# Kernel tuning notes

Hardware: AMD Instinct MI355X
Metric: run time of the kernel (lower is better)

## Reference

```python
import jax, jax.numpy as jnp
import numpy as np

N = 50000
E = 800000
NFEAT = 128
NHID = 32
HEADS = 8
NCLASS = 40


def _gat_conv(x, src, dst, W, att_src, att_dst, bias, concat):
    # x: [N, Fin]; W: [Fin, H*C]; att_*: [H, C]; bias: [H*C] or [C]
    n = x.shape[0]
    H, C = att_src.shape
    h = (x @ W).reshape(n, H, C)                      # [N,H,C]
    a_src = (h * att_src[None]).sum(-1)               # [N,H]
    a_dst = (h * att_dst[None]).sum(-1)               # [N,H]
    e = jax.nn.leaky_relu(a_src[src] + a_dst[dst], 0.2)  # [E,H]
    # edge softmax over incoming edges of each dst node
    m = jax.ops.segment_max(e, dst, num_segments=n)   # [N,H]
    e = jnp.exp(e - m[dst])
    s = jax.ops.segment_sum(e, dst, num_segments=n)   # [N,H]
    alpha = e / (s[dst] + 1e-16)                      # [E,H]
    msg = h[src] * alpha[:, :, None]                  # [E,H,C]
    out = jax.ops.segment_sum(msg, dst, num_segments=n)  # [N,H,C]
    if concat:
        out = out.reshape(n, H * C)
    else:
        out = out.mean(axis=1)
    return out + bias


def setup_inputs() -> dict:
    key = jax.random.key(0)
    ks = jax.random.split(key, 10)
    x = jax.random.normal(ks[0], (N, NFEAT), dtype=jnp.float32)
    edge_index = jax.random.randint(ks[1], (2, E), 0, N, dtype=jnp.int64)
    sc = 1.0 / np.sqrt(NFEAT)
    W1 = jax.random.uniform(ks[2], (NFEAT, HEADS * NHID), jnp.float32, -sc, sc)
    a1_src = jax.random.uniform(ks[3], (HEADS, NHID), jnp.float32, -sc, sc)
    a1_dst = jax.random.uniform(ks[4], (HEADS, NHID), jnp.float32, -sc, sc)
    b1 = jnp.zeros((HEADS * NHID,), jnp.float32)
    sc2 = 1.0 / np.sqrt(HEADS * NHID)
    W2 = jax.random.uniform(ks[5], (HEADS * NHID, NCLASS), jnp.float32, -sc2, sc2)
    a2_src = jax.random.uniform(ks[6], (1, NCLASS), jnp.float32, -sc2, sc2)
    a2_dst = jax.random.uniform(ks[7], (1, NCLASS), jnp.float32, -sc2, sc2)
    b2 = jnp.zeros((NCLASS,), jnp.float32)
    return {"x": x, "edge_index": edge_index, "W1": W1, "a1_src": a1_src,
            "a1_dst": a1_dst, "b1": b1, "W2": W2, "a2_src": a2_src,
            "a2_dst": a2_dst, "b2": b2}


def reference(x, edge_index, W1, a1_src, a1_dst, b1, W2, a2_src, a2_dst, b2):
    n = x.shape[0]
    loop = jnp.arange(n, dtype=edge_index.dtype)
    src = jnp.concatenate([edge_index[0], loop])  # add self-loops (PyG default)
    dst = jnp.concatenate([edge_index[1], loop])
    # dropout layers are identity in eval mode
    h = jax.nn.elu(_gat_conv(x, src, dst, W1, a1_src, a1_dst, b1, concat=True))
    out = _gat_conv(h, src, dst, W2, a2_src, a2_dst, b2, concat=False)
    return jax.nn.log_softmax(out, axis=1)
```

## Files before the change

kernel.cpp:

```cpp
#include <hip/hip_runtime.h>
#include <math.h>

#define NFEAT  128
#define HC     256
#define HEADS  8
#define NHID   32
#define NCLASS 40

typedef unsigned int  uint;
typedef unsigned short ushort;
typedef unsigned char uchar;

typedef __attribute__((ext_vector_type(8))) short bf16x8;
typedef __attribute__((ext_vector_type(4))) float f32x4;

union U8 { uint4 u; bf16x8 v; };

__device__ __forceinline__ uint f2bf1(float f) {
    uint b = __float_as_uint(f);
    b += 0x7FFFu + ((b >> 16) & 1u);
    return b >> 16;
}
__device__ __forceinline__ uint packbf(float lo, float hi) {
    return f2bf1(lo) | (f2bf1(hi) << 16);
}
__device__ __forceinline__ float bflo(uint u) { return __uint_as_float(u << 16); }
__device__ __forceinline__ float bfhi(uint u) { return __uint_as_float(u & 0xFFFF0000u); }

__device__ __forceinline__ uchar f2fp8(float v) {
    return (uchar)(__builtin_amdgcn_cvt_pk_fp8_f32(v, v, 0, false) & 0xFF);
}
__device__ __forceinline__ float fp8tof(uint byte) {
    auto v2 = __builtin_amdgcn_cvt_pk_f32_fp8((int)byte, false);
    return v2[0];
}


#define HU 8
#define PREPB 23
__global__ __launch_bounds__(256)
void k_hist_prep(const int* __restrict__ dst, int E, int* deg,
                 int* __restrict__ rank,
                 const float* __restrict__ W1,
                 const float* __restrict__ attS, const float* __restrict__ attD,
                 const float* __restrict__ W2,
                 const float* __restrict__ a2sw, const float* __restrict__ a2dw,
                 ushort* __restrict__ Wb1, ushort* __restrict__ Wb2) {
    int blk = blockIdx.x;
    int t = threadIdx.x;
    if (blk >= PREPB) {
        int tid = (blk - PREPB) * 256 + t;
        int stride = (gridDim.x - PREPB) * 256;
#pragma unroll
        for (int j = 0; j < HU; ++j) {
            int i = tid + j * stride;
            if (i < E) rank[i] = atomicAdd(&deg[dst[i]], 1);
        }
        return;
    }
    float f[8];
    if (blk < 17) {
        int g = blk * 256 + t;
        int lane = g & 63;
        int step = (g >> 6) & 3;
        int tile = g >> 8;
        int k0 = step * 32 + (lane >> 4) * 8;
        if (tile < 16) {
            int ncol = tile * 16 + (lane & 15);
#pragma unroll
            for (int j = 0; j < 8; ++j) f[j] = W1[(size_t)(k0 + j) * HC + ncol];
        } else {
            int cc = lane & 15;
            int h = cc & 7;
            const float* av = (cc < 8) ? attS : attD;
#pragma unroll
            for (int j = 0; j < 8; ++j) {
                const float* wr = W1 + (size_t)(k0 + j) * HC + h * 32;
                float s = 0.f;
#pragma unroll
                for (int c = 0; c < 32; ++c) s += wr[c] * av[h * 32 + c];
                f[j] = s;
            }
        }
        uint4 o;
        o.x = packbf(f[0], f[1]);
        o.y = packbf(f[2], f[3]);
        o.z = packbf(f[4], f[5]);
        o.w = packbf(f[6], f[7]);
        *(uint4*)(Wb1 + (size_t)g * 8) = o;
    } else {
        int g = (blk - 17) * 256 + t;
        if (g >= 3 * 8 * 64) return;
        int lane = g & 63;
        int ks = (g >> 6) & 7;
        int nt = g >> 9;
        int cc = lane & 15;
        int ncol = nt * 16 + cc;
        int k0 = ks * 32 + (lane >> 4) * 8;
        if (ncol < NCLASS) {
#pragma unroll
            for (int j = 0; j < 8; ++j) f[j] = W2[(size_t)(k0 + j) * NCLASS + ncol];
        } else if (ncol <= 41) {
            const float* av = (ncol == 40) ? a2sw : a2dw;
#pragma unroll
            for (int j = 0; j < 8; ++j) {
                const float* wr = W2 + (size_t)(k0 + j) * NCLASS;
                float s = 0.f;
#pragma unroll
                for (int c = 0; c < NCLASS; ++c) s += wr[c] * av[c];
                f[j] = s;
            }
        } else {
#pragma unroll
            for (int j = 0; j < 8; ++j) f[j] = 0.f;
        }
        uint4 o;
        o.x = packbf(f[0], f[1]);
        o.y = packbf(f[2], f[3]);
        o.z = packbf(f[4], f[5]);
        o.w = packbf(f[6], f[7]);
        *(uint4*)(Wb2 + (size_t)g * 8) = o;
    }
}

__global__ void k_blocksum(const int* __restrict__ deg, int n, int* bsum) {
    __shared__ int lds[256];
    int b = blockIdx.x, t = threadIdx.x;
    int i = b * 256 + t;
    lds[t] = (i < n) ? deg[i] + 1 : 0;
    __syncthreads();
    for (int off = 128; off >= 1; off >>= 1) {
        if (t < off) lds[t] += lds[t + off];
        __syncthreads();
    }
    if (t == 0) bsum[b] = lds[0];
}

__global__ void k_mkptr(const int* __restrict__ deg, const int* __restrict__ bsum,
                        int n, int* ptr) {
    __shared__ int lds[256];
    __shared__ int base_s;
    int b = blockIdx.x, t = threadIdx.x;
    int p = 0;
    for (int i = t; i < b; i += 256) p += bsum[i];
    lds[t] = p;
    __syncthreads();
    for (int off = 128; off >= 1; off >>= 1) {
        if (t < off) lds[t] += lds[t + off];
        __syncthreads();
    }
    if (t == 0) base_s = lds[0];
    __syncthreads();
    int i = b * 256 + t;
    int v = (i < n) ? deg[i] + 1 : 0;
    lds[t] = v;
    __syncthreads();
    for (int off = 1; off < 256; off <<= 1) {
        int u = (t >= off) ? lds[t - off] : 0;
        __syncthreads();
        lds[t] += u;
        __syncthreads();
    }
    int excl = lds[t] - v + base_s;
    if (i < n) {
        ptr[i] = excl;
        if (i == n - 1) ptr[n] = excl + v;
    }
}

#define SU 4
__global__ __launch_bounds__(256)
void k_scatter_gemm1(const int* __restrict__ srcE, const int* __restrict__ dstE,
                     const int* __restrict__ rank, const int* __restrict__ ptr,
                     int E, int n, int* __restrict__ srcs, int scb,
                     const float* __restrict__ x, const ushort* __restrict__ Wb,
                     uchar* __restrict__ h1f8, float* __restrict__ a1x) {
    __shared__ uint Xs[64 * 68];
    int t = threadIdx.x;
    if (blockIdx.x < scb) {
        int tid = blockIdx.x * 256 + t;
        int stride = scb * 256;
        int tot = E + n;
#pragma unroll
        for (int j = 0; j < SU; ++j) {
            int i = tid + j * stride;
            if (i >= tot) continue;
            if (i < E) {
                int d = dstE[i];
                srcs[ptr[d] + rank[i]] = srcE[i];
            } else {
                int v = i - E;
                srcs[ptr[v + 1] - 1] = v;
            }
        }
        return;
    }
    int lane = t & 63;
    int w = t >> 6;
    int n0 = (blockIdx.x - scb) * 64;

#pragma unroll
    for (int j = 0; j < 8; ++j) {
        int f4 = t + j * 256;
        int node = f4 >> 5;
        int k4 = (f4 & 31) * 4;
        int gn = n0 + node;
        float4 v = make_float4(0.f, 0.f, 0.f, 0.f);
        if (gn < n) v = *(const float4*)(x + (size_t)gn * NFEAT + k4);
        uint2 pk;
        pk.x = packbf(v.x, v.y);
        pk.y = packbf(v.z, v.w);
        *(uint2*)(Xs + node * 68 + (k4 >> 1)) = pk;
    }
    __syncthreads();

    int m = lane & 15;
    int q4 = (lane >> 4) * 4;
    bf16x8 Af[4];
#pragma unroll
    for (int ks = 0; ks < 4; ++ks) {
        U8 a;
        a.u = *(const uint4*)(Xs + (w * 16 + m) * 68 + ks * 16 + q4);
        Af[ks] = a.v;
    }
    __syncthreads();

    f32x4 acc[17];
#pragma unroll
    for (int i = 0; i < 17; ++i) acc[i] = (f32x4){0.f, 0.f, 0.f, 0.f};

    const bf16x8* Bf = (const bf16x8*)Wb;
#pragma unroll
    for (int ks = 0; ks < 4; ++ks) {
#pragma unroll
        for (int nt = 0; nt < 17; ++nt) {
            bf16x8 bv = Bf[(size_t)(nt * 4 + ks) * 64 + lane];
            acc[nt] = __builtin_amdgcn_mfma_f32_16x16x32_bf16(Af[ks], bv, acc[nt], 0, 0, 0);
        }
    }

    int cc = lane & 15;
    int r0 = (lane >> 4) * 4;

#pragma unroll
    for (int r = 0; r < 4; ++r) {
        int gn = n0 + w * 16 + r0 + r;
        if (gn < n) a1x[(size_t)gn * 16 + cc] = acc[16][r];
    }

    uchar* CsB = (uchar*)Xs;
#pragma unroll
    for (int nt = 0; nt < 16; ++nt) {
#pragma unroll
        for (int r = 0; r < 4; ++r)
            CsB[(w * 16 + r0 + r) * 272 + nt * 16 + cc] = f2fp8(acc[nt][r]);
    }
    __syncthreads();

    int node_local = t >> 2;
    int q = t & 3;
    int gn = n0 + node_local;
    if (gn < n) {
        const uchar* crow = CsB + node_local * 272 + q * 64;
        uchar* hp = h1f8 + (size_t)gn * HC + q * 64;
#pragma unroll
        for (int i = 0; i < 4; ++i)
            *(uint4*)(hp + i * 16) = *(const uint4*)(crow + i * 16);
    }
}

__global__ __launch_bounds__(256)
void k_agg1(const uint* __restrict__ h1u, const float* __restrict__ a1x,
            const float* __restrict__ b1,
            const int* __restrict__ ptr, const int* __restrict__ srcs,
            int n, ushort* __restrict__ hgb) {
    int wid = blockIdx.x * 4 + (threadIdx.x >> 6);
    if (wid >= n) return;
    int lane = threadIdx.x & 63;
    int h = lane >> 3;
    float adn = a1x[(size_t)wid * 16 + 8 + h];
    int beg = __builtin_amdgcn_readfirstlane(ptr[wid]);
    int end = __builtin_amdgcn_readfirstlane(ptr[wid + 1]);
    float m = -INFINITY, s = 0.f;
    float4 acc = make_float4(0.f, 0.f, 0.f, 0.f);

    int i = beg;
    for (; i + 8 <= end; i += 8) {
        int sn[8];
#pragma unroll
        for (int j = 0; j < 8; ++j) sn[j] = __builtin_amdgcn_readfirstlane(srcs[i + j]);
        float av[8];
        uint hv[8];
#pragma unroll
        for (int j = 0; j < 8; ++j) av[j] = a1x[(size_t)sn[j] * 16 + h];
#pragma unroll
        for (int j = 0; j < 8; ++j)
            hv[j] = h1u[(size_t)sn[j] * 64 + lane];
        float e[8];
#pragma unroll
        for (int j = 0; j < 8; ++j) {
            float a = av[j] + adn;
            e[j] = (a > 0.f) ? a : 0.2f * a;
        }
        float mn = m;
#pragma unroll
        for (int j = 0; j < 8; ++j) mn = fmaxf(mn, e[j]);
        float corr = __expf(m - mn);
        float p[8];
#pragma unroll
        for (int j = 0; j < 8; ++j) p[j] = __expf(e[j] - mn);
        float ps = 0.f;
#pragma unroll
        for (int j = 0; j < 8; ++j) ps += p[j];
        s = s * corr + ps;
        float cx = acc.x * corr, cy = acc.y * corr, cz = acc.z * corr, cw = acc.w * corr;
#pragma unroll
        for (int j = 0; j < 8; ++j) {
            auto lo = __builtin_amdgcn_cvt_pk_f32_fp8((int)hv[j], false);
            auto hi = __builtin_amdgcn_cvt_pk_f32_fp8((int)hv[j], true);
            cx += p[j] * lo[0];
            cy += p[j] * lo[1];
            cz += p[j] * hi[0];
            cw += p[j] * hi[1];
        }
        acc = make_float4(cx, cy, cz, cw);
        m = mn;
    }
    if (i < end) {
        int sn[8];
        bool val[8];
#pragma unroll
        for (int j = 0; j < 8; ++j) {
            int idx = i + j;
            val[j] = idx < end;
            sn[j] = __builtin_amdgcn_readfirstlane(srcs[val[j] ? idx : end - 1]);
        }
        float av[8];
        uint hv[8];
#pragma unroll
        for (int j = 0; j < 8; ++j) av[j] = a1x[(size_t)sn[j] * 16 + h];
#pragma unroll
        for (int j = 0; j < 8; ++j)
            hv[j] = h1u[(size_t)sn[j] * 64 + lane];
        float e[8];
#pragma unroll
        for (int j = 0; j < 8; ++j) {
            float a = av[j] + adn;
            e[j] = val[j] ? ((a > 0.f) ? a : 0.2f * a) : -INFINITY;
        }
        float mn = m;
#pragma unroll
        for (int j = 0; j < 8; ++j) mn = fmaxf(mn, e[j]);
        float corr = __expf(m - mn);
        float p[8];
#pragma unroll
        for (int j = 0; j < 8; ++j) p[j] = __expf(e[j] - mn);
        float ps = 0.f;
#pragma unroll
        for (int j = 0; j < 8; ++j) ps += p[j];
        s = s * corr + ps;
        float cx = acc.x * corr, cy = acc.y * corr, cz = acc.z * corr, cw = acc.w * corr;
#pragma unroll
        for (int j = 0; j < 8; ++j) {
            auto lo = __builtin_amdgcn_cvt_pk_f32_fp8((int)hv[j], false);
            auto hi = __builtin_amdgcn_cvt_pk_f32_fp8((int)hv[j], true);
            cx += p[j] * lo[0];
            cy += p[j] * lo[1];
            cz += p[j] * hi[0];
            cw += p[j] * hi[1];
        }
        acc = make_float4(cx, cy, cz, cw);
        m = mn;
    }

    float inv = 1.f / (s + 1e-16f);
    float4 bv = *(const float4*)(b1 + lane * 4);
    float4 o;
    o.x = acc.x * inv + bv.x;
    o.y = acc.y * inv + bv.y;
    o.z = acc.z * inv + bv.z;
    o.w = acc.w * inv + bv.w;
    o.x = (o.x > 0.f) ? o.x : (__expf(o.x) - 1.f);
    o.y = (o.y > 0.f) ? o.y : (__expf(o.y) - 1.f);
    o.z = (o.z > 0.f) ? o.z : (__expf(o.z) - 1.f);
    o.w = (o.w > 0.f) ? o.w : (__expf(o.w) - 1.f);
    uint2 ov;
    ov.x = packbf(o.x, o.y);
    ov.y = packbf(o.z, o.w);
    *(uint2*)(hgb + (size_t)wid * HC + lane * 4) = ov;
}

__global__ __launch_bounds__(256)
void k_gemm2(const ushort* __restrict__ hgb, const ushort* __restrict__ Wb2,
             int n, uchar* __restrict__ h2f8) {
    __shared__ uint Xs[64 * 132];
    int t = threadIdx.x;
    int lane = t & 63;
    int w = t >> 6;
    int n0 = blockIdx.x * 64;

#pragma unroll
    for (int j = 0; j < 8; ++j) {
        int g = t + j * 256;
        int node = g >> 5;
        int u4 = g & 31;
        int gn = n0 + node;
        uint4 v = make_uint4(0u, 0u, 0u, 0u);
        if (gn < n) v = *(const uint4*)(hgb + (size_t)gn * HC + u4 * 8);
        *(uint4*)(Xs + node * 132 + u4 * 4) = v;
    }
    __syncthreads();

    int m = lane & 15;
    int q4 = (lane >> 4) * 4;
    bf16x8 Af[8];
#pragma unroll
    for (int ks = 0; ks < 8; ++ks) {
        U8 a;
        a.u = *(const uint4*)(Xs + (w * 16 + m) * 132 + ks * 16 + q4);
        Af[ks] = a.v;
    }
    __syncthreads();

    f32x4 acc[3];
#pragma unroll
    for (int i = 0; i < 3; ++i) acc[i] = (f32x4){0.f, 0.f, 0.f, 0.f};

    const bf16x8* Bf = (const bf16x8*)Wb2;
#pragma unroll
    for (int ks = 0; ks < 8; ++ks) {
#pragma unroll
        for (int nt = 0; nt < 3; ++nt) {
            bf16x8 bv = Bf[(size_t)(nt * 8 + ks) * 64 + lane];
            acc[nt] = __builtin_amdgcn_mfma_f32_16x16x32_bf16(Af[ks], bv, acc[nt], 0, 0, 0);
        }
    }

    int cc = lane & 15;
    int r0 = (lane >> 4) * 4;

    uchar* CsB = (uchar*)Xs;
#pragma unroll
    for (int nt = 0; nt < 2; ++nt) {
#pragma unroll
        for (int r = 0; r < 4; ++r)
            CsB[(w * 16 + r0 + r) * 64 + nt * 16 + cc] = f2fp8(acc[nt][r]);
    }
#pragma unroll
    for (int r = 0; r < 4; ++r) {
        int row = (w * 16 + r0 + r) * 64;
        if (cc < 8)       CsB[row + 32 + cc] = f2fp8(acc[2][r]);
        else if (cc == 8) *(float*)(CsB + row + 40) = acc[2][r];
        else if (cc == 9) *(float*)(CsB + row + 44) = acc[2][r];
        else if (cc == 10) *(uint*)(CsB + row + 48) = 0u;
        else if (cc == 11) *(uint*)(CsB + row + 52) = 0u;
        else if (cc == 12) *(uint*)(CsB + row + 56) = 0u;
        else if (cc == 13) *(uint*)(CsB + row + 60) = 0u;
    }
    __syncthreads();

    int node_local = t >> 2;
    int q = t & 3;
    int gn = n0 + node_local;
    if (gn < n)
        *(uint4*)(h2f8 + (size_t)gn * 64 + q * 16) =
            *(const uint4*)(CsB + node_local * 64 + q * 16);
}

__global__ __launch_bounds__(256)
void k_agg2(const uchar* __restrict__ h2f8, const float* __restrict__ b2,
            const int* __restrict__ ptr, const int* __restrict__ srcs,
            int n, float* __restrict__ out) {
    int wid = blockIdx.x * 4 + (threadIdx.x >> 6);
    if (wid >= n) return;
    int lane = threadIdx.x & 63;
    bool live = lane < NCLASS;
    int col = live ? lane : 0;
    float adn = *(const float*)(h2f8 + (size_t)wid * 64 + 44);
    int beg = __builtin_amdgcn_readfirstlane(ptr[wid]);
    int end = __builtin_amdgcn_readfirstlane(ptr[wid + 1]);
    float m = -INFINITY, s = 0.f, acc = 0.f;

    int i = beg;
    for (; i + 8 <= end; i += 8) {
        int sn[8];
#pragma unroll
        for (int j = 0; j < 8; ++j) sn[j] = __builtin_amdgcn_readfirstlane(srcs[i + j]);
        float av[8];
        uint hb[8];
#pragma unroll
        for (int j = 0; j < 8; ++j)
            av[j] = *(const float*)(h2f8 + (size_t)sn[j] * 64 + 40);
#pragma unroll
        for (int j = 0; j < 8; ++j)
            hb[j] = h2f8[(size_t)sn[j] * 64 + col];
        float e[8];
#pragma unroll
        for (int j = 0; j < 8; ++j) {
            float a = av[j] + adn;
            e[j] = (a > 0.f) ? a : 0.2f * a;
        }
        float mn = m;
#pragma unroll
        for (int j = 0; j < 8; ++j) mn = fmaxf(mn, e[j]);
        float corr = __expf(m - mn);
        float p[8];
#pragma unroll
        for (int j = 0; j < 8; ++j) p[j] = __expf(e[j] - mn);
        float ps = 0.f, pa = 0.f;
#pragma unroll
        for (int j = 0; j < 8; ++j) { ps += p[j]; pa += p[j] * fp8tof(hb[j]); }
        s = s * corr + ps;
        acc = acc * corr + pa;
        m = mn;
    }
    if (i < end) {
        int sn[8];
        bool val[8];
#pragma unroll
        for (int j = 0; j < 8; ++j) {
            int idx = i + j;
            val[j] = idx < end;
            sn[j] = __builtin_amdgcn_readfirstlane(srcs[val[j] ? idx : end - 1]);
        }
        float av[8];
        uint hb[8];
#pragma unroll
        for (int j = 0; j < 8; ++j)
            av[j] = *(const float*)(h2f8 + (size_t)sn[j] * 64 + 40);
#pragma unroll
        for (int j = 0; j < 8; ++j)
            hb[j] = h2f8[(size_t)sn[j] * 64 + col];
        float e[8];
#pragma unroll
        for (int j = 0; j < 8; ++j) {
            float a = av[j] + adn;
            e[j] = val[j] ? ((a > 0.f) ? a : 0.2f * a) : -INFINITY;
        }
        float mn = m;
#pragma unroll
        for (int j = 0; j < 8; ++j) mn = fmaxf(mn, e[j]);
        float corr = __expf(m - mn);
        float p[8];
#pragma unroll
        for (int j = 0; j < 8; ++j) p[j] = __expf(e[j] - mn);
        float ps = 0.f, pa = 0.f;
#pragma unroll
        for (int j = 0; j < 8; ++j) { ps += p[j]; pa += p[j] * fp8tof(hb[j]); }
        s = s * corr + ps;
        acc = acc * corr + pa;
        m = mn;
    }

    float val0 = acc / (s + 1e-16f) + (live ? b2[lane] : 0.f);
    float vmax = live ? val0 : -INFINITY;
#pragma unroll
    for (int msk = 1; msk < 64; msk <<= 1) vmax = fmaxf(vmax, __shfl_xor(vmax, msk, 64));
    float ex = live ? __expf(val0 - vmax) : 0.f;
#pragma unroll
    for (int msk = 1; msk < 64; msk <<= 1) ex += __shfl_xor(ex, msk, 64);
    float res = val0 - vmax - __logf(ex);
    if (live) out[(size_t)wid * NCLASS + lane] = res;
}

extern "C" void kernel_launch(void* const* d_in, const int* in_sizes, int n_in,
                              void* d_out, int out_size, void* d_ws, size_t ws_size,
                              hipStream_t stream) {
    const float* x    = (const float*)d_in[0];
    const int*   ei   = (const int*)  d_in[1];
    const float* W1   = (const float*)d_in[2];
    const float* attS = (const float*)d_in[3];
    const float* attD = (const float*)d_in[4];
    const float* b1   = (const float*)d_in[5];
    const float* W2   = (const float*)d_in[6];
    const float* a2sw = (const float*)d_in[7];
    const float* a2dw = (const float*)d_in[8];
    const float* b2   = (const float*)d_in[9];

    int n = in_sizes[0] / NFEAT;
    int E = in_sizes[1] / 2;
    const int* srcE = ei;
    const int* dstE = ei + E;
    int nb = (n + 255) / 256;
    int mblocks = (n + 63) / 64;

    char* p = (char*)d_ws;
    auto alloc = [&](size_t bytes) {
        char* r = p;
        p += (bytes + 255) & ~(size_t)255;
        return r;
    };
    uchar*  h1f8 = (uchar*)alloc((size_t)n * HC);
    ushort* hgb  = (ushort*)alloc((size_t)n * HC * 2);
    uchar*  h2f8 = (uchar*)alloc((size_t)n * 64);
    ushort* Wb1  = (ushort*)alloc((size_t)17 * 4 * 64 * 8 * 2);
    ushort* Wb2  = (ushort*)alloc((size_t)3 * 8 * 64 * 8 * 2);
    float* a1x = (float*)alloc((size_t)n * 16 * 4);
    int* deg  = (int*)alloc((size_t)n * 4);
    int* rank = (int*)alloc((size_t)E * 4);
    int* bsum = (int*)alloc((size_t)nb * 4);
    int* ptr  = (int*)alloc((size_t)(n + 1) * 4);
    int* srcs = (int*)alloc((size_t)(E + n) * 4);

    int tot = E + n;
    int histb = (E + 256 * HU - 1) / (256 * HU);
    int scb = (tot + 256 * SU - 1) / (256 * SU);
    hipMemsetAsync(deg, 0, (size_t)n * 4, stream);
    k_hist_prep<<<PREPB + histb, 256, 0, stream>>>(dstE, E, deg, rank,
                                                   W1, attS, attD, W2, a2sw, a2dw,
                                                   Wb1, Wb2);
    k_blocksum<<<nb, 256, 0, stream>>>(deg, n, bsum);
    k_mkptr<<<nb, 256, 0, stream>>>(deg, bsum, n, ptr);

    k_scatter_gemm1<<<scb + mblocks, 256, 0, stream>>>(
        srcE, dstE, rank, ptr, E, n, srcs, scb, x, Wb1, h1f8, a1x);

    k_agg1<<<(n + 3) / 4, 256, 0, stream>>>((const uint*)h1f8, a1x, b1,
                                            ptr, srcs, n, hgb);
    k_gemm2<<<(n + 63) / 64, 256, 0, stream>>>(hgb, Wb2, n, h2f8);
    k_agg2<<<(n + 3) / 4, 256, 0, stream>>>(h2f8, b2, ptr, srcs, n, (float*)d_out);
}
```

Measured before the change: 251.0 us.

## Distribute edge softmax across lanes with bpermute reductions and exp2 prescaling

```diff
diff --git a/kernel.cpp b/kernel.cpp
--- a/kernel.cpp
+++ b/kernel.cpp
@@ -7,6 +7,8 @@
 #define NHID   32
 #define NCLASS 40
 
+#define INV_LN2 1.44269504088896340736f
+
 typedef unsigned int  uint;
 typedef unsigned short ushort;
 typedef unsigned char uchar;
@@ -33,6 +35,10 @@
 __device__ __forceinline__ float fp8tof(uint byte) {
     auto v2 = __builtin_amdgcn_cvt_pk_f32_fp8((int)byte, false);
     return v2[0];
+}
+
+__device__ __forceinline__ float bperm(int addr, float v) {
+    return __int_as_float(__builtin_amdgcn_ds_bpermute(addr, __float_as_int(v)));
 }
 
 
@@ -79,7 +85,7 @@
                 float s = 0.f;
 #pragma unroll
                 for (int c = 0; c < 32; ++c) s += wr[c] * av[h * 32 + c];
-                f[j] = s;
+                f[j] = s * INV_LN2;
             }
         }
         uint4 o;
@@ -108,7 +114,7 @@
                 float s = 0.f;
 #pragma unroll
                 for (int c = 0; c < NCLASS; ++c) s += wr[c] * av[c];
-                f[j] = s;
+                f[j] = s * INV_LN2;
             }
         } else {
 #pragma unroll
@@ -277,109 +283,69 @@
     int wid = blockIdx.x * 4 + (threadIdx.x >> 6);
     if (wid >= n) return;
     int lane = threadIdx.x & 63;
-    int h = lane >> 3;
-    float adn = a1x[(size_t)wid * 16 + 8 + h];
+    int vj = lane >> 3;
+    int hh = lane & 7;
+    int hacc = lane >> 3;
+    float adn = a1x[(size_t)wid * 16 + 8 + hh];
+    const char* a1xb = (const char*)a1x;
+    const char* srcsb = (const char*)srcs;
+    int ax8  = (lane ^ 8)  << 2;
+    int ax16 = (lane ^ 16) << 2;
+    int ax32 = (lane ^ 32) << 2;
+    int bpc  = hacc << 2;
+    int bpp[8];
+#pragma unroll
+    for (int j = 0; j < 8; ++j) bpp[j] = ((j << 3) + hacc) << 2;
+
     int beg = __builtin_amdgcn_readfirstlane(ptr[wid]);
     int end = __builtin_amdgcn_readfirstlane(ptr[wid + 1]);
     float m = -INFINITY, s = 0.f;
     float4 acc = make_float4(0.f, 0.f, 0.f, 0.f);
 
-    int i = beg;
-    for (; i + 8 <= end; i += 8) {
-        int sn[8];
-#pragma unroll
-        for (int j = 0; j < 8; ++j) sn[j] = __builtin_amdgcn_readfirstlane(srcs[i + j]);
-        float av[8];
-        uint hv[8];
-#pragma unroll
-        for (int j = 0; j < 8; ++j) av[j] = a1x[(size_t)sn[j] * 16 + h];
-#pragma unroll
-        for (int j = 0; j < 8; ++j)
-            hv[j] = h1u[(size_t)sn[j] * 64 + lane];
-        float e[8];
+    for (int i = beg; i < end; i += 8) {
+        int idx = i + vj;
+        bool valid = idx < end;
+        int ci = valid ? idx : (end - 1);
+        int sv = *(const int*)(srcsb + ((uint)ci << 2));
+        float av = *(const float*)(a1xb + ((uint)sv << 6) + ((uint)hh << 2));
+        float a = av + adn;
+        float e = fmaxf(a, 0.2f * a);
+        e = valid ? e : -INFINITY;
+        float em = fmaxf(e, bperm(ax8, e));
+        em = fmaxf(em, bperm(ax16, em));
+        em = fmaxf(em, bperm(ax32, em));
+        float mn = fmaxf(m, em);
+        float corr = __builtin_exp2f(m - mn);
+        float p = __builtin_exp2f(e - mn);
+        float ps = p + bperm(ax8, p);
+        ps += bperm(ax16, ps);
+        ps += bperm(ax32, ps);
+        s = s * corr + ps;
+        m = mn;
+        float corr_a = bperm(bpc, corr);
+        acc.x *= corr_a; acc.y *= corr_a; acc.z *= corr_a; acc.w *= corr_a;
 #pragma unroll
         for (int j = 0; j < 8; ++j) {
-            float a = av[j] + adn;
-            e[j] = (a > 0.f) ? a : 0.2f * a;
-        }
-        float mn = m;
-#pragma unroll
-        for (int j = 0; j < 8; ++j) mn = fmaxf(mn, e[j]);
-        float corr = __expf(m - mn);
-        float p[8];
-#pragma unroll
-        for (int j = 0; j < 8; ++j) p[j] = __expf(e[j] - mn);
-        float ps = 0.f;
-#pragma unroll
-        for (int j = 0; j < 8; ++j) ps += p[j];
-        s = s * corr + ps;
-        float cx = acc.x * corr, cy = acc.y * corr, cz = acc.z * corr, cw = acc.w * corr;
-#pragma unroll
-        for (int j = 0; j < 8; ++j) {
-            auto lo = __builtin_amdgcn_cvt_pk_f32_fp8((int)hv[j], false);
-            auto hi = __builtin_amdgcn_cvt_pk_f32_fp8((int)hv[j], true);
-            cx += p[j] * lo[0];
-            cy += p[j] * lo[1];
-            cz += p[j] * hi[0];
-            cw += p[j] * hi[1];
-        }
-        acc = make_float4(cx, cy, cz, cw);
-        m = mn;
-    }
-    if (i < end) {
-        int sn[8];
-        bool val[8];
-#pragma unroll
-        for (int j = 0; j < 8; ++j) {
-            int idx = i + j;
-            val[j] = idx < end;
-            sn[j] = __builtin_amdgcn_readfirstlane(srcs[val[j] ? idx : end - 1]);
-        }
-        float av[8];
-        uint hv[8];
-#pragma unroll
-        for (int j = 0; j < 8; ++j) av[j] = a1x[(size_t)sn[j] * 16 + h];
-#pragma unroll
-        for (int j = 0; j < 8; ++j)
-            hv[j] = h1u[(size_t)sn[j] * 64 + lane];
-        float e[8];
-#pragma unroll
-        for (int j = 0; j < 8; ++j) {
-            float a = av[j] + adn;
-            e[j] = val[j] ? ((a > 0.f) ? a : 0.2f * a) : -INFINITY;
-        }
-        float mn = m;
-#pragma unroll
-        for (int j = 0; j < 8; ++j) mn = fmaxf(mn, e[j]);
-        float corr = __expf(m - mn);
-        float p[8];
-#pragma unroll
-        for (int j = 0; j < 8; ++j) p[j] = __expf(e[j] - mn);
-        float ps = 0.f;
-#pragma unroll
-        for (int j = 0; j < 8; ++j) ps += p[j];
-        s = s * corr + ps;
-        float cx = acc.x * corr, cy = acc.y * corr, cz = acc.z * corr, cw = acc.w * corr;
-#pragma unroll
-        for (int j = 0; j < 8; ++j) {
-            auto lo = __builtin_amdgcn_cvt_pk_f32_fp8((int)hv[j], false);
-            auto hi = __builtin_amdgcn_cvt_pk_f32_fp8((int)hv[j], true);
-            cx += p[j] * lo[0];
-            cy += p[j] * lo[1];
-            cz += p[j] * hi[0];
-            cw += p[j] * hi[1];
-        }
-        acc = make_float4(cx, cy, cz, cw);
-        m = mn;
+            int snj = __builtin_amdgcn_readlane(sv, 8 * j);
+            uint hv = h1u[(size_t)snj * 64 + lane];
+            float pj = bperm(bpp[j], p);
+            auto lo = __builtin_amdgcn_cvt_pk_f32_fp8((int)hv, false);
+            auto hi = __builtin_amdgcn_cvt_pk_f32_fp8((int)hv, true);
+            acc.x += pj * lo[0];
+            acc.y += pj * lo[1];
+            acc.z += pj * hi[0];
+            acc.w += pj * hi[1];
+        }
     }
 
     float inv = 1.f / (s + 1e-16f);
+    float inv_a = bperm(bpc, inv);
     float4 bv = *(const float4*)(b1 + lane * 4);
     float4 o;
-    o.x = acc.x * inv + bv.x;
-    o.y = acc.y * inv + bv.y;
-    o.z = acc.z * inv + bv.z;
-    o.w = acc.w * inv + bv.w;
+    o.x = acc.x * inv_a + bv.x;
+    o.y = acc.y * inv_a + bv.y;
+    o.z = acc.z * inv_a + bv.z;
+    o.w = acc.w * inv_a + bv.w;
     o.x = (o.x > 0.f) ? o.x : (__expf(o.x) - 1.f);
     o.y = (o.y > 0.f) ? o.y : (__expf(o.y) - 1.f);
     o.z = (o.z > 0.f) ? o.z : (__expf(o.z) - 1.f);
@@ -474,82 +440,51 @@
     int wid = blockIdx.x * 4 + (threadIdx.x >> 6);
     if (wid >= n) return;
     int lane = threadIdx.x & 63;
+    int vj = lane & 7;
     bool live = lane < NCLASS;
     int col = live ? lane : 0;
-    float adn = *(const float*)(h2f8 + (size_t)wid * 64 + 44);
+    const char* h2b = (const char*)h2f8;
+    const char* srcsb = (const char*)srcs;
+    float adn = *(const float*)(h2b + (size_t)wid * 64 + 44);
+    int ax1 = (lane ^ 1) << 2;
+    int ax2 = (lane ^ 2) << 2;
+    int ax4 = (lane ^ 4) << 2;
+    int bpj[8];
+#pragma unroll
+    for (int j = 0; j < 8; ++j) bpj[j] = j << 2;
+
     int beg = __builtin_amdgcn_readfirstlane(ptr[wid]);
     int end = __builtin_amdgcn_readfirstlane(ptr[wid + 1]);
     float m = -INFINITY, s = 0.f, acc = 0.f;
 
-    int i = beg;
-    for (; i + 8 <= end; i += 8) {
-        int sn[8];
-#pragma unroll
-        for (int j = 0; j < 8; ++j) sn[j] = __builtin_amdgcn_readfirstlane(srcs[i + j]);
-        float av[8];
-        uint hb[8];
-#pragma unroll
-        for (int j = 0; j < 8; ++j)
-            av[j] = *(const float*)(h2f8 + (size_t)sn[j] * 64 + 40);
-#pragma unroll
-        for (int j = 0; j < 8; ++j)
-            hb[j] = h2f8[(size_t)sn[j] * 64 + col];
-        float e[8];
+    for (int i = beg; i < end; i += 8) {
+        int idx = i + vj;
+        bool valid = idx < end;
+        int ci = valid ? idx : (end - 1);
+        int sv = *(const int*)(srcsb + ((uint)ci << 2));
+        float av = *(const float*)(h2b + ((uint)sv << 6) + 40u);
+        float a = av + adn;
+        float e = fmaxf(a, 0.2f * a);
+        e = valid ? e : -INFINITY;
+        float em = fmaxf(e, bperm(ax1, e));
+        em = fmaxf(em, bperm(ax2, em));
+        em = fmaxf(em, bperm(ax4, em));
+        float mn = fmaxf(m, em);
+        float corr = __builtin_exp2f(m - mn);
+        float p = __builtin_exp2f(e - mn);
+        float ps = p + bperm(ax1, p);
+        ps += bperm(ax2, ps);
+        ps += bperm(ax4, ps);
+        s = s * corr + ps;
+        acc = acc * corr;
+        m = mn;
 #pragma unroll
         for (int j = 0; j < 8; ++j) {
-            float a = av[j] + adn;
-            e[j] = (a > 0.f) ? a : 0.2f * a;
-        }
-        float mn = m;
-#pragma unroll
-        for (int j = 0; j < 8; ++j) mn = fmaxf(mn, e[j]);
-        float corr = __expf(m - mn);
-        float p[8];
-#pragma unroll
-        for (int j = 0; j < 8; ++j) p[j] = __expf(e[j] - mn);
-        float ps = 0.f, pa = 0.f;
-#pragma unroll
-        for (int j = 0; j < 8; ++j) { ps += p[j]; pa += p[j] * fp8tof(hb[j]); }
-        s = s * corr + ps;
-        acc = acc * corr + pa;
-        m = mn;
-    }
-    if (i < end) {
-        int sn[8];
-        bool val[8];
-#pragma unroll
-        for (int j = 0; j < 8; ++j) {
-            int idx = i + j;
-            val[j] = idx < end;
-            sn[j] = __builtin_amdgcn_readfirstlane(srcs[val[j] ? idx : end - 1]);
-        }
-        float av[8];
-        uint hb[8];
-#pragma unroll
-        for (int j = 0; j < 8; ++j)
-            av[j] = *(const float*)(h2f8 + (size_t)sn[j] * 64 + 40);
-#pragma unroll
-        for (int j = 0; j < 8; ++j)
-            hb[j] = h2f8[(size_t)sn[j] * 64 + col];
-        float e[8];
-#pragma unroll
-        for (int j = 0; j < 8; ++j) {
-            float a = av[j] + adn;
-            e[j] = val[j] ? ((a > 0.f) ? a : 0.2f * a) : -INFINITY;
-        }
-        float mn = m;
-#pragma unroll
-        for (int j = 0; j < 8; ++j) mn = fmaxf(mn, e[j]);
-        float corr = __expf(m - mn);
-        float p[8];
-#pragma unroll
-        for (int j = 0; j < 8; ++j) p[j] = __expf(e[j] - mn);
-        float ps = 0.f, pa = 0.f;
-#pragma unroll
-        for (int j = 0; j < 8; ++j) { ps += p[j]; pa += p[j] * fp8tof(hb[j]); }
-        s = s * corr + ps;
-        acc = acc * corr + pa;
-        m = mn;
+            int snj = __builtin_amdgcn_readlane(sv, j);
+            uint hb = h2f8[(size_t)snj * 64 + col];
+            float pj = bperm(bpj[j], p);
+            acc += pj * fp8tof(hb);
+        }
     }
 
     float val0 = acc / (s + 1e-16f) + (live ? b2[lane] : 0.f);
```

After: 244.2 us. 2.7% less time.
